# Performance work log

Measured on AMD Instinct MI355X. Metric: run time of the kernel, lower is better.

## Reference

```python
import jax, jax.numpy as jnp
import numpy as np


def _shift_gather(x, s, axis):
    """Gather x shifted by integer offset s along `axis`, zero outside bounds.

    Matches deform_conv2d's zero-padding bilinear-corner semantics: each
    integer corner outside [0, n) contributes zero.
    """
    n = x.shape[axis]
    idx = jnp.arange(n) + s                      # traced integer shift
    valid = (idx >= 0) & (idx < n)
    g = jnp.take(x, jnp.clip(idx, 0, n - 1), axis=axis)
    bshape = [1] * x.ndim
    bshape[axis] = n
    return g * valid.reshape(bshape).astype(x.dtype)


def _axial_deform_dw(x, taps_w, r_val, axis):
    """Depthwise 1D conv along `axis` with fractional (learned) dilation.

    For tap k_pos in [-P, P], deform_conv2d samples at base + k_pos + k_pos*(r-1)
    = base + k_pos * r, i.e. a constant fractional shift per tap, realized via
    bilinear interpolation between the two neighboring integer rows/cols.
    taps_w: (C, K) depthwise weights along the given spatial axis.
    """
    K = taps_w.shape[1]
    P = K // 2
    out = jnp.zeros_like(x)
    for i in range(K):
        k_pos = i - P
        delta = k_pos * r_val                    # fractional sampling shift (traced)
        d0f = jnp.floor(delta)
        frac = (delta - d0f).astype(x.dtype)
        d0 = d0f.astype(jnp.int32)
        s0 = _shift_gather(x, d0, axis)
        s1 = _shift_gather(x, d0 + 1, axis)
        samp = (1.0 - frac) * s0 + frac * s1     # bilinear along the axis
        out = out + samp * taps_w[:, i][None, :, None, None]
    return out


def reference(x, weight_h, weight_w, r):
    # r is clamped to >= 1 as in the torch module
    r_val = jnp.clip(r, 1.0)
    wh = weight_h[:, 0, :, 0]                    # (C, kh) vertical taps
    ww = weight_w[:, 0, 0, :]                    # (C, kw) horizontal taps
    out_h = _axial_deform_dw(x, wh, r_val, axis=2)  # deform conv along H
    out_w = _axial_deform_dw(x, ww, r_val, axis=3)  # deform conv along W
    return x + out_h + out_w


def setup_inputs() -> dict:
    key = jax.random.key(0)
    k0, k1, k2 = jax.random.split(key, 3)
    B, C, H, W, KH, KW = 8, 128, 224, 224, 7, 7
    x = jax.random.normal(k0, (B, C, H, W), dtype=jnp.float32)
    # kaiming_normal fan_out scale ~ sqrt(2 / (C * K))
    weight_h = jax.random.normal(k1, (C, 1, KH, 1), dtype=jnp.float32) * np.sqrt(2.0 / (C * KH))
    weight_w = jax.random.normal(k2, (C, 1, 1, KW), dtype=jnp.float32) * np.sqrt(2.0 / (C * KW))
    r = jnp.asarray(1.7, dtype=jnp.float32)      # learned dilation parameter
    return {"x": x, "weight_h": weight_h, "weight_w": weight_w, "r": r}
```

## Files before the change

kernel.cpp:

```cpp
#include <hip/hip_runtime.h>
#include <stdint.h>


namespace {
constexpr int B = 8, C = 128, H = 224, W = 224;
constexpr int KT = 7;
constexpr int M  = 6;
constexpr int NT = 2 * M + 1;
constexpr int TH = 32;
constexpr int NTPB = 7;
constexpr int SROWS = TH + 2 * M;
constexpr int WQ = W / 4;
constexpr int BLOCK = 512;
constexpr int RPT = 4;
constexpr int WROWS = RPT + 2 * M;
constexpr int RSTRIDE = 224;
constexpr int BUF_FLOATS = SROWS * RSTRIDE;
constexpr int LDS_FLOATS = 2 * BUF_FLOATS;
constexpr int ZOFF = 2 * C * NT;
}

typedef __attribute__((address_space(3))) uint32_t lds_u32;
typedef __attribute__((address_space(1))) const uint32_t gbl_u32;

__global__ void taps_kernel(const float* __restrict__ wh, const float* __restrict__ ww,
                            const float* __restrict__ r, float* __restrict__ taps) {
    int c = threadIdx.x;
    if (c >= C) return;
    taps[ZOFF + c]     = 0.f;
    taps[ZOFF + C + c] = 0.f;
    float rv = fmaxf(r[0], 1.0f);
    float eh[NT], ew[NT];
    for (int j = 0; j < NT; ++j) { eh[j] = 0.f; ew[j] = 0.f; }
    for (int i = 0; i < KT; ++i) {
        float kpos  = (float)(i - KT / 2);
        float delta = kpos * rv;
        float d0f   = floorf(delta);
        float fr    = delta - d0f;
        int   j0    = (int)d0f + M;
        float whv = wh[c * KT + i];
        float wwv = ww[c * KT + i];
        if (j0 >= 0 && j0 < NT)         { eh[j0]   += (1.f - fr) * whv; ew[j0]   += (1.f - fr) * wwv; }
        if (j0 + 1 >= 0 && j0 + 1 < NT) { eh[j0+1] += fr * whv;         ew[j0+1] += fr * wwv; }
    }
    for (int j = 0; j < NT; ++j) {
        taps[c * NT + j]          = eh[j];
        taps[C * NT + c * NT + j] = ew[j];
    }
}

__global__ __launch_bounds__(BLOCK) void deform_axial_kernel(
    const float* __restrict__ x, const float* __restrict__ taps,
    float* __restrict__ out) {
    __shared__ float lds[LDS_FLOATS];

    const int p     = blockIdx.x;
    const int c     = p & (C - 1);
    const int tid   = threadIdx.x;
    const int wave  = tid >> 6;
    const int lane  = tid & 63;
    const bool producer = (wave == 7);

    const long base = (long)p * (H * W);
    const float* __restrict__ xp = x + base;

    float eh[NT], ew[NT];
    const float* __restrict__ ehp = taps + c * NT;
    const float* __restrict__ ewp = taps + C * NT + c * NT;
#pragma unroll
    for (int j = 0; j < NT; ++j) { eh[j] = ehp[j]; ew[j] = ewp[j]; }
    const float ws6 = ew[6] + 1.0f;
    asm volatile("s_waitcnt vmcnt(0)" ::: "memory");

    const float* zbase = taps + ZOFF + lane * 4;
    float* const buf0 = lds;
    float* const buf1 = lds + BUF_FLOATS;

    auto STAGE = [&](float* bufb, int t) {
        const int h0 = t * TH;
#pragma unroll
        for (int row = 0; row < SROWS; ++row) {
            const int grow = h0 - M + row;
            const bool vr  = (unsigned)grow < (unsigned)H;
            const float* src = vr ? (xp + grow * W + lane * 4) : zbase;
            float* dst = bufb + row * RSTRIDE;
            if (lane < 56) {
                __builtin_amdgcn_global_load_lds((gbl_u32*)src, (lds_u32*)dst, 16, 0, 0);
            }
        }
    };

    auto BAR = []() {
        asm volatile("" ::: "memory");
        __builtin_amdgcn_s_barrier();
        asm volatile("" ::: "memory");
    };

    const int cq = tid % WQ;
    const int rg = tid / WQ;
    const int r0 = rg * RPT;
    const float4 zero4 = make_float4(0.f, 0.f, 0.f, 0.f);

    auto COMPUTE = [&](const float* ldsb, int t) {
        const int h0 = t * TH;
        float4 acc[RPT];
#pragma unroll
        for (int k = 0; k < RPT; ++k) acc[k] = zero4;

#pragma unroll
        for (int s = 0; s < WROWS; ++s) {
            const float4 q = *reinterpret_cast<const float4*>(&ldsb[(r0 + s) * RSTRIDE + cq * 4]);

#pragma unroll
            for (int k = 0; k < RPT; ++k) {
                const int j = s - k;
                if (j >= 0 && j < NT) {
                    const float wgt = eh[j];
                    acc[k].x = fmaf(wgt, q.x, acc[k].x);
                    acc[k].y = fmaf(wgt, q.y, acc[k].y);
                    acc[k].z = fmaf(wgt, q.z, acc[k].z);
                    acc[k].w = fmaf(wgt, q.w, acc[k].w);
                }
            }

            if (s >= M && s < M + RPT) {
                const int k = s - M;
                const float* crow = &ldsb[(r0 + s) * RSTRIDE];
                float4& a = acc[k];

                {
                    const float4 qd = (cq >= 2) ? *reinterpret_cast<const float4*>(crow + (cq - 2) * 4) : zero4;
                    a.x = fmaf(ew[0], qd.z, a.x);
                    a.x = fmaf(ew[1], qd.w, a.x);
                    a.y = fmaf(ew[0], qd.w, a.y);
                }
                {
                    const float4 qd = (cq >= 1) ? *reinterpret_cast<const float4*>(crow + (cq - 1) * 4) : zero4;
                    a.x = fmaf(ew[2], qd.x, a.x); a.y = fmaf(ew[1], qd.x, a.y); a.z = fmaf(ew[0], qd.x, a.z);
                    a.x = fmaf(ew[3], qd.y, a.x); a.y = fmaf(ew[2], qd.y, a.y); a.z = fmaf(ew[1], qd.y, a.z); a.w = fmaf(ew[0], qd.y, a.w);
                    a.x = fmaf(ew[4], qd.z, a.x); a.y = fmaf(ew[3], qd.z, a.y); a.z = fmaf(ew[2], qd.z, a.z); a.w = fmaf(ew[1], qd.z, a.w);
                    a.x = fmaf(ew[5], qd.w, a.x); a.y = fmaf(ew[4], qd.w, a.y); a.z = fmaf(ew[3], qd.w, a.z); a.w = fmaf(ew[2], qd.w, a.w);
                }
                {
                    a.x = fmaf(ws6,   q.x, a.x); a.y = fmaf(ew[5], q.x, a.y); a.z = fmaf(ew[4], q.x, a.z); a.w = fmaf(ew[3], q.x, a.w);
                    a.x = fmaf(ew[7], q.y, a.x); a.y = fmaf(ws6,   q.y, a.y); a.z = fmaf(ew[5], q.y, a.z); a.w = fmaf(ew[4], q.y, a.w);
                    a.x = fmaf(ew[8], q.z, a.x); a.y = fmaf(ew[7], q.z, a.y); a.z = fmaf(ws6,   q.z, a.z); a.w = fmaf(ew[5], q.z, a.w);
                    a.x = fmaf(ew[9], q.w, a.x); a.y = fmaf(ew[8], q.w, a.y); a.z = fmaf(ew[7], q.w, a.z); a.w = fmaf(ws6,   q.w, a.w);
                }
                {
                    const float4 qd = (cq <= WQ - 2) ? *reinterpret_cast<const float4*>(crow + (cq + 1) * 4) : zero4;
                    a.x = fmaf(ew[10], qd.x, a.x); a.y = fmaf(ew[9],  qd.x, a.y); a.z = fmaf(ew[8],  qd.x, a.z); a.w = fmaf(ew[7],  qd.x, a.w);
                    a.x = fmaf(ew[11], qd.y, a.x); a.y = fmaf(ew[10], qd.y, a.y); a.z = fmaf(ew[9],  qd.y, a.z); a.w = fmaf(ew[8],  qd.y, a.w);
                    a.x = fmaf(ew[12], qd.z, a.x); a.y = fmaf(ew[11], qd.z, a.y); a.z = fmaf(ew[10], qd.z, a.z); a.w = fmaf(ew[9],  qd.z, a.w);
                                                   a.y = fmaf(ew[12], qd.w, a.y); a.z = fmaf(ew[11], qd.w, a.z); a.w = fmaf(ew[10], qd.w, a.w);
                }
                {
                    const float4 qd = (cq <= WQ - 3) ? *reinterpret_cast<const float4*>(crow + (cq + 2) * 4) : zero4;
                    a.z = fmaf(ew[12], qd.x, a.z);
                    a.w = fmaf(ew[11], qd.x, a.w);
                    a.w = fmaf(ew[12], qd.y, a.w);
                }
            }
        }

        float* outp = out + base + (long)(h0 + r0) * W + cq * 4;
#pragma unroll
        for (int k = 0; k < RPT; ++k) {
            *reinterpret_cast<float4*>(outp + k * W) = acc[k];
        }
    };

    if (producer) {
        STAGE(buf0, 0);
        asm volatile("s_waitcnt vmcnt(0)" ::: "memory");
    }
    BAR();

#pragma unroll
    for (int t = 0; t < NTPB; ++t) {
        if (producer) {
            if (t + 1 < NTPB) {
                STAGE((t & 1) ? buf0 : buf1, t + 1);
                asm volatile("s_waitcnt vmcnt(0)" ::: "memory");
            }
        } else {
            COMPUTE((t & 1) ? buf1 : buf0, t);
        }
        BAR();
    }
}

extern "C" void kernel_launch(void* const* d_in, const int* in_sizes, int n_in,
                              void* d_out, int out_size, void* d_ws, size_t ws_size,
                              hipStream_t stream) {
    const float* x  = (const float*)d_in[0];
    const float* wh = (const float*)d_in[1];
    const float* ww = (const float*)d_in[2];
    const float* r  = (const float*)d_in[3];
    float* out  = (float*)d_out;
    float* taps = (float*)d_ws;

    hipLaunchKernelGGL(taps_kernel, dim3(1), dim3(C), 0, stream, wh, ww, r, taps);
    hipLaunchKernelGGL(deform_axial_kernel, dim3(B * C), dim3(BLOCK),
                       0, stream, x, taps, out);
}
```

Baseline: 94.73 us.

## Split each image plane into two width halves with haloed LDS tiles

Each block now handles half the width of a (b,c) plane, staging 32 float4 columns (28 output plus 2-column halos on each side) into LDS, so the grid doubles and each block shrinks to 320 threads. Halo columns outside the image are zero-filled at staging time, which removes the per-thread boundary conditionals in the horizontal convolution. The aim is more blocks per CU and less LDS per block for better occupancy and latency hiding. The cost is reading the halo columns twice and having one idle wave in each block.

```diff
diff --git a/kernel.cpp b/kernel.cpp
--- a/kernel.cpp
+++ b/kernel.cpp
@@ -10,12 +10,14 @@
 constexpr int TH = 32;
 constexpr int NTPB = 7;
 constexpr int SROWS = TH + 2 * M;
-constexpr int WQ = W / 4;
-constexpr int BLOCK = 512;
+constexpr int OQ = 28;
+constexpr int SQ = 32;
+constexpr int BLOCK = 320;
+constexpr int NCONS = 224;
 constexpr int RPT = 4;
 constexpr int WROWS = RPT + 2 * M;
-constexpr int RSTRIDE = 224;
-constexpr int BUF_FLOATS = SROWS * RSTRIDE;
+constexpr int RFLOATS = SQ * 4;
+constexpr int BUF_FLOATS = SROWS * RFLOATS;
 constexpr int LDS_FLOATS = 2 * BUF_FLOATS;
 constexpr int ZOFF = 2 * C * NT;
 }
@@ -54,12 +56,15 @@
     float* __restrict__ out) {
     __shared__ float lds[LDS_FLOATS];
 
-    const int p     = blockIdx.x;
+    const int bid   = blockIdx.x;
+    const int p     = bid >> 1;
+    const int whf   = bid & 1;
+    const int qb0   = whf * OQ - 2;
     const int c     = p & (C - 1);
     const int tid   = threadIdx.x;
     const int wave  = tid >> 6;
     const int lane  = tid & 63;
-    const bool producer = (wave == 7);
+    const bool producer = (wave == 4);
 
     const long base = (long)p * (H * W);
     const float* __restrict__ xp = x + base;
@@ -78,13 +83,15 @@
 
     auto STAGE = [&](float* bufb, int t) {
         const int h0 = t * TH;
+        const int sq = qb0 + lane;
+        const bool cv = (unsigned)sq < (unsigned)(W / 4);
 #pragma unroll
         for (int row = 0; row < SROWS; ++row) {
             const int grow = h0 - M + row;
-            const bool vr  = (unsigned)grow < (unsigned)H;
-            const float* src = vr ? (xp + grow * W + lane * 4) : zbase;
-            float* dst = bufb + row * RSTRIDE;
-            if (lane < 56) {
+            const bool vr  = cv & ((unsigned)grow < (unsigned)H);
+            const float* src = vr ? (xp + grow * W + sq * 4) : zbase;
+            float* dst = bufb + row * RFLOATS;
+            if (lane < SQ) {
                 __builtin_amdgcn_global_load_lds((gbl_u32*)src, (lds_u32*)dst, 16, 0, 0);
             }
         }
@@ -96,8 +103,8 @@
         asm volatile("" ::: "memory");
     };
 
-    const int cq = tid % WQ;
-    const int rg = tid / WQ;
+    const int cq = tid % OQ;
+    const int rg = tid / OQ;
     const int r0 = rg * RPT;
     const float4 zero4 = make_float4(0.f, 0.f, 0.f, 0.f);
 
@@ -109,7 +116,8 @@
 
 #pragma unroll
         for (int s = 0; s < WROWS; ++s) {
-            const float4 q = *reinterpret_cast<const float4*>(&ldsb[(r0 + s) * RSTRIDE + cq * 4]);
+            const float* rowp = &ldsb[(r0 + s) * RFLOATS];
+            const float4 q = *reinterpret_cast<const float4*>(rowp + (cq + 2) * 4);
 
 #pragma unroll
             for (int k = 0; k < RPT; ++k) {
@@ -125,17 +133,16 @@
 
             if (s >= M && s < M + RPT) {
                 const int k = s - M;
-                const float* crow = &ldsb[(r0 + s) * RSTRIDE];
                 float4& a = acc[k];
 
                 {
-                    const float4 qd = (cq >= 2) ? *reinterpret_cast<const float4*>(crow + (cq - 2) * 4) : zero4;
+                    const float4 qd = *reinterpret_cast<const float4*>(rowp + (cq + 0) * 4);
                     a.x = fmaf(ew[0], qd.z, a.x);
                     a.x = fmaf(ew[1], qd.w, a.x);
                     a.y = fmaf(ew[0], qd.w, a.y);
                 }
                 {
-                    const float4 qd = (cq >= 1) ? *reinterpret_cast<const float4*>(crow + (cq - 1) * 4) : zero4;
+                    const float4 qd = *reinterpret_cast<const float4*>(rowp + (cq + 1) * 4);
                     a.x = fmaf(ew[2], qd.x, a.x); a.y = fmaf(ew[1], qd.x, a.y); a.z = fmaf(ew[0], qd.x, a.z);
                     a.x = fmaf(ew[3], qd.y, a.x); a.y = fmaf(ew[2], qd.y, a.y); a.z = fmaf(ew[1], qd.y, a.z); a.w = fmaf(ew[0], qd.y, a.w);
                     a.x = fmaf(ew[4], qd.z, a.x); a.y = fmaf(ew[3], qd.z, a.y); a.z = fmaf(ew[2], qd.z, a.z); a.w = fmaf(ew[1], qd.z, a.w);
@@ -148,14 +155,14 @@
                     a.x = fmaf(ew[9], q.w, a.x); a.y = fmaf(ew[8], q.w, a.y); a.z = fmaf(ew[7], q.w, a.z); a.w = fmaf(ws6,   q.w, a.w);
                 }
                 {
-                    const float4 qd = (cq <= WQ - 2) ? *reinterpret_cast<const float4*>(crow + (cq + 1) * 4) : zero4;
+                    const float4 qd = *reinterpret_cast<const float4*>(rowp + (cq + 3) * 4);
                     a.x = fmaf(ew[10], qd.x, a.x); a.y = fmaf(ew[9],  qd.x, a.y); a.z = fmaf(ew[8],  qd.x, a.z); a.w = fmaf(ew[7],  qd.x, a.w);
                     a.x = fmaf(ew[11], qd.y, a.x); a.y = fmaf(ew[10], qd.y, a.y); a.z = fmaf(ew[9],  qd.y, a.z); a.w = fmaf(ew[8],  qd.y, a.w);
                     a.x = fmaf(ew[12], qd.z, a.x); a.y = fmaf(ew[11], qd.z, a.y); a.z = fmaf(ew[10], qd.z, a.z); a.w = fmaf(ew[9],  qd.z, a.w);
                                                    a.y = fmaf(ew[12], qd.w, a.y); a.z = fmaf(ew[11], qd.w, a.z); a.w = fmaf(ew[10], qd.w, a.w);
                 }
                 {
-                    const float4 qd = (cq <= WQ - 3) ? *reinterpret_cast<const float4*>(crow + (cq + 2) * 4) : zero4;
+                    const float4 qd = *reinterpret_cast<const float4*>(rowp + (cq + 4) * 4);
                     a.z = fmaf(ew[12], qd.x, a.z);
                     a.w = fmaf(ew[11], qd.x, a.w);
                     a.w = fmaf(ew[12], qd.y, a.w);
@@ -163,7 +170,7 @@
             }
         }
 
-        float* outp = out + base + (long)(h0 + r0) * W + cq * 4;
+        float* outp = out + base + (long)(h0 + r0) * W + (whf * OQ + cq) * 4;
 #pragma unroll
         for (int k = 0; k < RPT; ++k) {
             *reinterpret_cast<float4*>(outp + k * W) = acc[k];
@@ -183,7 +190,7 @@
                 STAGE((t & 1) ? buf0 : buf1, t + 1);
                 asm volatile("s_waitcnt vmcnt(0)" ::: "memory");
             }
-        } else {
+        } else if (tid < NCONS) {
             COMPUTE((t & 1) ? buf1 : buf0, t);
         }
         BAR();
@@ -201,6 +208,6 @@
     float* taps = (float*)d_ws;
 
     hipLaunchKernelGGL(taps_kernel, dim3(1), dim3(C), 0, stream, wh, ww, r, taps);
-    hipLaunchKernelGGL(deform_axial_kernel, dim3(B * C), dim3(BLOCK),
+    hipLaunchKernelGGL(deform_axial_kernel, dim3(2 * B * C), dim3(BLOCK),
                        0, stream, x, taps, out);
 }
```

Measured after the change: 105.4 us. +11.2%, slower.
